# Kernel optimization log

Hardware: AMD Instinct MI355X
Metric: run time of the kernel (lower is better)

The kernel has to match this reference:

```python
import jax, jax.numpy as jnp
import numpy as np

H, W = 4096, 4096
KH, KW = 15, 15


def setup_inputs() -> dict:
    key = jax.random.key(0)
    k1, k2 = jax.random.split(key)
    x = jax.random.normal(k1, (H, W), dtype=jnp.float32)
    weight = jax.random.normal(k2, (KH, KW), dtype=jnp.float32)
    bias = jnp.zeros((1,), dtype=jnp.float32)
    return {"x": x, "weight": weight, "bias": bias}


def reference(x, weight, bias):
    # corr2d: valid cross-correlation of 2D x with 2D kernel, output [H-KH+1, W-KW+1]
    # lax conv with NCHW/OIHW layout computes cross-correlation (no kernel flip),
    # identical to the torch per-pixel slice-multiply-sum loop.
    out = jax.lax.conv_general_dilated(
        x[None, None, :, :],            # [1,1,H,W]
        weight[None, None, :, :],       # [1,1,KH,KW]
        window_strides=(1, 1),
        padding="VALID",
    )[0, 0]                             # [H-KH+1, W-KW+1]
    return out + bias  # bias is shape [1], broadcasts like torch
```

## Files before the change

kernel.cpp:

```cpp
#include <hip/hip_runtime.h>


#define HIN 4096
#define WIN 4096
#define KH 15
#define KW 15
#define OH (HIN - KH + 1)
#define OW (WIN - KW + 1)

#define BX 64
#define BY 64
#define XROWS (BY + KH - 1)
#define XCOLS 80
#define LDSW 88
#define NSH (XROWS * LDSW)
#define NB4 (XCOLS / 4)
#define NITEM (XROWS * NB4)

typedef short bf16x8 __attribute__((ext_vector_type(8)));
typedef float f32x4  __attribute__((ext_vector_type(4)));

static __device__ inline short f2bf(float f) {
    unsigned u = __float_as_uint(f);
    u += 0x7fffu + ((u >> 16) & 1u);
    return (short)(u >> 16);
}

__global__ void conv2d_btab(const float* __restrict__ w, short* __restrict__ btab) {
    const int e = blockIdx.x * 256 + threadIdx.x;
    if (e >= KH * 64) return;
    const int kh = e >> 6;
    const int L  = e & 63;
    const int n  = L & 15;
    const int q  = L >> 4;
    bf16x8 bv;
#pragma unroll
    for (int j = 0; j < 8; ++j) {
        const int d = q * 8 + j - n;
        bv[j] = (d >= 0 && d < KW) ? f2bf(w[kh * KW + d]) : (short)0;
    }
    *reinterpret_cast<bf16x8*>(&btab[(size_t)e * 8]) = bv;
}

__global__ __launch_bounds__(256, 8)
void conv2d_mfma(const float* __restrict__ x,
                 const short* __restrict__ btab,
                 const float* __restrict__ bias,
                 float* __restrict__ out) {
    __shared__ short lds[NSH];

    const int tid = threadIdx.x;
    const int ox0 = blockIdx.x * BX;
    const int oy0 = blockIdx.y * BY;

    if (ox0 + XCOLS <= WIN && oy0 + XROWS <= HIN) {
        float4 v[7];
#pragma unroll
        for (int i = 0; i < 7; ++i) {
            const int f = tid + 256 * i;
            if (f < NITEM) {
                const int r  = f / NB4;
                const int c4 = (f - r * NB4) * 4;
                v[i] = *reinterpret_cast<const float4*>(&x[(size_t)(oy0 + r) * WIN + ox0 + c4]);
            }
        }
#pragma unroll
        for (int i = 0; i < 7; ++i) {
            const int f = tid + 256 * i;
            if (f < NITEM) {
                const int r  = f / NB4;
                const int c4 = (f - r * NB4) * 4;
                short4 s;
                s.x = f2bf(v[i].x); s.y = f2bf(v[i].y);
                s.z = f2bf(v[i].z); s.w = f2bf(v[i].w);
                *reinterpret_cast<short4*>(&lds[r * LDSW + c4]) = s;
            }
        }
    } else {
        for (int f = tid; f < NITEM; f += 256) {
            const int r  = f / NB4;
            const int c4 = (f - r * NB4) * 4;
            int gy = oy0 + r;
            if (gy > HIN - 1) gy = HIN - 1;
            const int gx = ox0 + c4;
            float4 v;
            if (gx + 3 <= WIN - 1) {
                v = *reinterpret_cast<const float4*>(&x[(size_t)gy * WIN + gx]);
            } else {
                const float* row = &x[(size_t)gy * WIN];
                const int x0 = (gx + 0 > WIN - 1) ? WIN - 1 : gx + 0;
                const int x1 = (gx + 1 > WIN - 1) ? WIN - 1 : gx + 1;
                const int x2 = (gx + 2 > WIN - 1) ? WIN - 1 : gx + 2;
                const int x3 = (gx + 3 > WIN - 1) ? WIN - 1 : gx + 3;
                v = make_float4(row[x0], row[x1], row[x2], row[x3]);
            }
            short4 s;
            s.x = f2bf(v.x); s.y = f2bf(v.y); s.z = f2bf(v.z); s.w = f2bf(v.w);
            *reinterpret_cast<short4*>(&lds[r * LDSW + c4]) = s;
        }
    }
    __syncthreads();

    const int lane = tid & 63;
    const int wv   = tid >> 6;
    const int m    = lane & 15;
    const int q    = lane >> 4;

    f32x4 acc[4];
#pragma unroll
    for (int t = 0; t < 4; ++t) acc[t] = (f32x4){0.f, 0.f, 0.f, 0.f};

    const short*  abase = &lds[(wv * 16 + m) * LDSW + q * 8];
    const bf16x8* bt    = reinterpret_cast<const bf16x8*>(btab) + lane;
#pragma unroll
    for (int kh = 0; kh < KH; ++kh) {
        const bf16x8 b = bt[kh * 64];
#pragma unroll
        for (int t = 0; t < 4; ++t) {
            const bf16x8 a =
                *reinterpret_cast<const bf16x8*>(abase + kh * LDSW + t * 16);
            acc[t] = __builtin_amdgcn_mfma_f32_16x16x32_bf16(a, b, acc[t], 0, 0, 0);
        }
    }

    const float b0 = bias[0];
    const int row0 = oy0 + wv * 16 + q * 4;
#pragma unroll
    for (int t = 0; t < 4; ++t) {
        const int col = ox0 + t * 16 + m;
        if (col < OW) {
#pragma unroll
            for (int r = 0; r < 4; ++r) {
                const int row = row0 + r;
                if (row < OH)
                    out[(size_t)row * OW + col] = acc[t][r] + b0;
            }
        }
    }
}

extern "C" void kernel_launch(void* const* d_in, const int* in_sizes, int n_in,
                              void* d_out, int out_size, void* d_ws, size_t ws_size,
                              hipStream_t stream) {
    const float* x    = (const float*)d_in[0];
    const float* w    = (const float*)d_in[1];
    const float* bias = (const float*)d_in[2];
    float* out        = (float*)d_out;
    short* btab       = (short*)d_ws;

    conv2d_btab<<<dim3((KH * 64 + 255) / 256), dim3(256), 0, stream>>>(w, btab);

    dim3 grid((OW + BX - 1) / BX, (OH + BY - 1) / BY);
    dim3 block(256);
    conv2d_mfma<<<grid, block, 0, stream>>>(x, btab, bias, out);
}
```

Measured before the change: 138.2 us.

## Double-buffer input tiles with async global-to-LDS loads across multiple row tiles

Each block now processes four output row tiles, strided across a grid of 16 in y. The next tile's fp32 input is prefetched into an LDS staging buffer with global_load_lds while the MFMA loop runs on the current bf16 buffer. After the stores, the staged data is converted into the alternate bf16 buffer, so global load latency overlaps with compute. This adds a large fp32 staging area to LDS and lowers launch bounds to 4, which cuts occupancy. The vmcnt(0) wait before conversion also waits on the outstanding output stores, which may limit how much overlap is actually achieved.

```diff
diff --git a/kernel.cpp b/kernel.cpp
--- a/kernel.cpp
+++ b/kernel.cpp
@@ -13,12 +13,20 @@
 #define XROWS (BY + KH - 1)
 #define XCOLS 80
 #define LDSW 88
-#define NSH (XROWS * LDSW)
+#define NSHB (XROWS * LDSW)
+#define NSTG (XROWS * XCOLS)
 #define NB4 (XCOLS / 4)
 #define NITEM (XROWS * NB4)
+#define TJ 4
+#define GRIDY 16
 
 typedef short bf16x8 __attribute__((ext_vector_type(8)));
 typedef float f32x4  __attribute__((ext_vector_type(4)));
+
+#define GLD_LDS16(gp, lp)                                                    \
+    __builtin_amdgcn_global_load_lds(                                        \
+        (const __attribute__((address_space(1))) void*)(gp),                 \
+        (__attribute__((address_space(3))) void*)(lp), 16, 0, 0)
 
 static __device__ inline short f2bf(float f) {
     unsigned u = __float_as_uint(f);
@@ -42,52 +50,65 @@
     *reinterpret_cast<bf16x8*>(&btab[(size_t)e * 8]) = bv;
 }
 
-__global__ __launch_bounds__(256, 8)
+__global__ __launch_bounds__(256, 4)
 void conv2d_mfma(const float* __restrict__ x,
                  const short* __restrict__ btab,
                  const float* __restrict__ bias,
                  float* __restrict__ out) {
-    __shared__ short lds[NSH];
+    __shared__ __align__(16) float stage[NSTG];
+    __shared__ __align__(16) short bufA[NSHB];
+    __shared__ __align__(16) short bufB[NSHB];
 
-    const int tid = threadIdx.x;
-    const int ox0 = blockIdx.x * BX;
-    const int oy0 = blockIdx.y * BY;
+    const int tid  = threadIdx.x;
+    const int lane = tid & 63;
+    const int wv   = tid >> 6;
+    const int ox0  = blockIdx.x * BX;
+    const bool xint = (ox0 + XCOLS <= WIN);
 
-    if (ox0 + XCOLS <= WIN && oy0 + XROWS <= HIN) {
-        float4 v[7];
+    auto dma_issue = [&](int iy0) {
 #pragma unroll
         for (int i = 0; i < 7; ++i) {
             const int f = tid + 256 * i;
             if (f < NITEM) {
                 const int r  = f / NB4;
                 const int c4 = (f - r * NB4) * 4;
-                v[i] = *reinterpret_cast<const float4*>(&x[(size_t)(oy0 + r) * WIN + ox0 + c4]);
+                int gy = iy0 + r;
+                if (gy > HIN - 1) gy = HIN - 1;
+                GLD_LDS16(&x[(size_t)gy * WIN + ox0 + c4], &stage[(size_t)f * 4]);
             }
         }
+        __builtin_amdgcn_sched_barrier(0);
+    };
+
+    auto convert = [&](short* buf) {
+        asm volatile("s_waitcnt vmcnt(0)" ::: "memory");
+        __builtin_amdgcn_sched_barrier(0);
 #pragma unroll
         for (int i = 0; i < 7; ++i) {
             const int f = tid + 256 * i;
             if (f < NITEM) {
                 const int r  = f / NB4;
                 const int c4 = (f - r * NB4) * 4;
+                const float4 v = *reinterpret_cast<const float4*>(&stage[(size_t)f * 4]);
                 short4 s;
-                s.x = f2bf(v[i].x); s.y = f2bf(v[i].y);
-                s.z = f2bf(v[i].z); s.w = f2bf(v[i].w);
-                *reinterpret_cast<short4*>(&lds[r * LDSW + c4]) = s;
+                s.x = f2bf(v.x); s.y = f2bf(v.y); s.z = f2bf(v.z); s.w = f2bf(v.w);
+                *reinterpret_cast<short4*>(&buf[r * LDSW + c4]) = s;
             }
         }
-    } else {
+    };
+
+    auto edge_stage = [&](int iy0, short* buf) {
         for (int f = tid; f < NITEM; f += 256) {
             const int r  = f / NB4;
             const int c4 = (f - r * NB4) * 4;
-            int gy = oy0 + r;
+            int gy = iy0 + r;
             if (gy > HIN - 1) gy = HIN - 1;
+            const float* row = &x[(size_t)gy * WIN];
             const int gx = ox0 + c4;
             float4 v;
             if (gx + 3 <= WIN - 1) {
-                v = *reinterpret_cast<const float4*>(&x[(size_t)gy * WIN + gx]);
+                v = *reinterpret_cast<const float4*>(&row[gx]);
             } else {
-                const float* row = &x[(size_t)gy * WIN];
                 const int x0 = (gx + 0 > WIN - 1) ? WIN - 1 : gx + 0;
                 const int x1 = (gx + 1 > WIN - 1) ? WIN - 1 : gx + 1;
                 const int x2 = (gx + 2 > WIN - 1) ? WIN - 1 : gx + 2;
@@ -96,45 +117,67 @@
             }
             short4 s;
             s.x = f2bf(v.x); s.y = f2bf(v.y); s.z = f2bf(v.z); s.w = f2bf(v.w);
-            *reinterpret_cast<short4*>(&lds[r * LDSW + c4]) = s;
+            *reinterpret_cast<short4*>(&buf[r * LDSW + c4]) = s;
         }
+    };
+
+    const int m = lane & 15;
+    const int q = lane >> 4;
+    const int aoff = (wv * 16 + m) * LDSW + q * 8;
+    const bf16x8* bt = reinterpret_cast<const bf16x8*>(btab) + lane;
+    const float b0 = bias[0];
+    const int by0 = blockIdx.y;
+
+    if (xint) {
+        dma_issue(by0 * BY);
+        convert(bufA);
+    } else {
+        edge_stage(by0 * BY, bufA);
     }
     __syncthreads();
 
-    const int lane = tid & 63;
-    const int wv   = tid >> 6;
-    const int m    = lane & 15;
-    const int q    = lane >> 4;
+#pragma unroll
+    for (int j = 0; j < TJ; ++j) {
+        const int oy0 = (by0 + GRIDY * j) * BY;
+        const short* cur = (j & 1) ? bufB : bufA;
+        short*       nxt = (j & 1) ? bufA : bufB;
 
-    f32x4 acc[4];
+        if (j + 1 < TJ && xint)
+            dma_issue((by0 + GRIDY * (j + 1)) * BY);
+
+        const short* abase = cur + aoff;
+        f32x4 acc[4];
 #pragma unroll
-    for (int t = 0; t < 4; ++t) acc[t] = (f32x4){0.f, 0.f, 0.f, 0.f};
+        for (int t = 0; t < 4; ++t) acc[t] = (f32x4){0.f, 0.f, 0.f, 0.f};
+#pragma unroll
+        for (int kh = 0; kh < KH; ++kh) {
+            const bf16x8 b = bt[kh * 64];
+#pragma unroll
+            for (int t = 0; t < 4; ++t) {
+                const bf16x8 a =
+                    *reinterpret_cast<const bf16x8*>(abase + kh * LDSW + t * 16);
+                acc[t] = __builtin_amdgcn_mfma_f32_16x16x32_bf16(a, b, acc[t], 0, 0, 0);
+            }
+        }
 
-    const short*  abase = &lds[(wv * 16 + m) * LDSW + q * 8];
-    const bf16x8* bt    = reinterpret_cast<const bf16x8*>(btab) + lane;
-#pragma unroll
-    for (int kh = 0; kh < KH; ++kh) {
-        const bf16x8 b = bt[kh * 64];
+        const int row0 = oy0 + wv * 16 + q * 4;
 #pragma unroll
         for (int t = 0; t < 4; ++t) {
-            const bf16x8 a =
-                *reinterpret_cast<const bf16x8*>(abase + kh * LDSW + t * 16);
-            acc[t] = __builtin_amdgcn_mfma_f32_16x16x32_bf16(a, b, acc[t], 0, 0, 0);
+            const int col = ox0 + t * 16 + m;
+            if (col < OW) {
+#pragma unroll
+                for (int r = 0; r < 4; ++r) {
+                    const int row = row0 + r;
+                    if (row < OH)
+                        out[(size_t)row * OW + col] = acc[t][r] + b0;
+                }
+            }
         }
-    }
 
-    const float b0 = bias[0];
-    const int row0 = oy0 + wv * 16 + q * 4;
-#pragma unroll
-    for (int t = 0; t < 4; ++t) {
-        const int col = ox0 + t * 16 + m;
-        if (col < OW) {
-#pragma unroll
-            for (int r = 0; r < 4; ++r) {
-                const int row = row0 + r;
-                if (row < OH)
-                    out[(size_t)row * OW + col] = acc[t][r] + b0;
-            }
+        if (j + 1 < TJ) {
+            if (xint) convert(nxt);
+            else      edge_stage((by0 + GRIDY * (j + 1)) * BY, nxt);
+            __syncthreads();
         }
     }
 }
@@ -150,7 +193,7 @@
 
     conv2d_btab<<<dim3((KH * 64 + 255) / 256), dim3(256), 0, stream>>>(w, btab);
 
-    dim3 grid((OW + BX - 1) / BX, (OH + BY - 1) / BY);
+    dim3 grid((OW + BX - 1) / BX, GRIDY);
     dim3 block(256);
     conv2d_mfma<<<grid, block, 0, stream>>>(x, btab, bias, out);
 }
```

Measured after the change: 157.4 us. 13.9% more time.

## Reshape conv tile to 16x256 outputs with waves split along columns

Applied to the files above, without the earlier changes.

Changes the block tile from 64x64 outputs to 16 rows by 256 columns, so each wave now covers a 64-column strip of the same 16 rows instead of its own 16-row band. The input halo per block becomes 30x272, which changes the ratio of halo to useful input and makes each row load a long contiguous run. The aim is better coalescing and fewer small partial row segments. In exchange, vertical halo overhead grows (30 rows loaded for 16 output rows versus 78 for 64), so total input traffic and LDS footprint per block shift.

```diff
diff --git a/kernel.cpp b/kernel.cpp
--- a/kernel.cpp
+++ b/kernel.cpp
@@ -8,14 +8,14 @@
 #define OH (HIN - KH + 1)
 #define OW (WIN - KW + 1)
 
-#define BX 64
-#define BY 64
-#define XROWS (BY + KH - 1)
-#define XCOLS 80
-#define LDSW 88
-#define NSH (XROWS * LDSW)
-#define NB4 (XCOLS / 4)
-#define NITEM (XROWS * NB4)
+#define BXO 256
+#define BYO 16
+#define XR (BYO + KH - 1)
+#define XC 272
+#define XC4 (XC / 4)
+#define LDSW 280
+#define NSH (XR * LDSW)
+#define NITEM (XR * XC4)
 
 typedef short bf16x8 __attribute__((ext_vector_type(8)));
 typedef float f32x4  __attribute__((ext_vector_type(4)));
@@ -50,26 +50,27 @@
     __shared__ short lds[NSH];
 
     const int tid = threadIdx.x;
-    const int ox0 = blockIdx.x * BX;
-    const int oy0 = blockIdx.y * BY;
+    const int ox0 = blockIdx.x * BXO;
+    const int oy0 = blockIdx.y * BYO;
+    const bool interior = (ox0 + XC <= WIN) && (oy0 + XR <= HIN);
 
-    if (ox0 + XCOLS <= WIN && oy0 + XROWS <= HIN) {
-        float4 v[7];
+    if (interior) {
+        float4 v[8];
 #pragma unroll
-        for (int i = 0; i < 7; ++i) {
+        for (int i = 0; i < 8; ++i) {
             const int f = tid + 256 * i;
             if (f < NITEM) {
-                const int r  = f / NB4;
-                const int c4 = (f - r * NB4) * 4;
+                const int r  = f / XC4;
+                const int c4 = (f - r * XC4) * 4;
                 v[i] = *reinterpret_cast<const float4*>(&x[(size_t)(oy0 + r) * WIN + ox0 + c4]);
             }
         }
 #pragma unroll
-        for (int i = 0; i < 7; ++i) {
+        for (int i = 0; i < 8; ++i) {
             const int f = tid + 256 * i;
             if (f < NITEM) {
-                const int r  = f / NB4;
-                const int c4 = (f - r * NB4) * 4;
+                const int r  = f / XC4;
+                const int c4 = (f - r * XC4) * 4;
                 short4 s;
                 s.x = f2bf(v[i].x); s.y = f2bf(v[i].y);
                 s.z = f2bf(v[i].z); s.w = f2bf(v[i].w);
@@ -78,8 +79,8 @@
         }
     } else {
         for (int f = tid; f < NITEM; f += 256) {
-            const int r  = f / NB4;
-            const int c4 = (f - r * NB4) * 4;
+            const int r  = f / XC4;
+            const int c4 = (f - r * XC4) * 4;
             int gy = oy0 + r;
             if (gy > HIN - 1) gy = HIN - 1;
             const int gx = ox0 + c4;
@@ -110,7 +111,7 @@
 #pragma unroll
     for (int t = 0; t < 4; ++t) acc[t] = (f32x4){0.f, 0.f, 0.f, 0.f};
 
-    const short*  abase = &lds[(wv * 16 + m) * LDSW + q * 8];
+    const short*  abase = &lds[m * LDSW + wv * 64 + q * 8];
     const bf16x8* bt    = reinterpret_cast<const bf16x8*>(btab) + lane;
 #pragma unroll
     for (int kh = 0; kh < KH; ++kh) {
@@ -124,10 +125,10 @@
     }
 
     const float b0 = bias[0];
-    const int row0 = oy0 + wv * 16 + q * 4;
+    const int row0 = oy0 + q * 4;
 #pragma unroll
     for (int t = 0; t < 4; ++t) {
-        const int col = ox0 + t * 16 + m;
+        const int col = ox0 + wv * 64 + t * 16 + m;
         if (col < OW) {
 #pragma unroll
             for (int r = 0; r < 4; ++r) {
@@ -150,7 +151,7 @@
 
     conv2d_btab<<<dim3((KH * 64 + 255) / 256), dim3(256), 0, stream>>>(w, btab);
 
-    dim3 grid((OW + BX - 1) / BX, (OH + BY - 1) / BY);
+    dim3 grid((OW + BXO - 1) / BXO, (OH + BYO - 1) / BYO);
     dim3 block(256);
     conv2d_mfma<<<grid, block, 0, stream>>>(x, btab, bias, out);
 }
```

Result: slower. 146.4 us (+6.0%).
